# Kernel tuning notes

Hardware: AMD Instinct MI355X
Metric: run time of the kernel (lower is better)

## Reference

```python
import jax, jax.numpy as jnp
import numpy as np

B, S, D, DIM = 8, 4096, 1024, 512  # batch, src nodes, dst nodes, feature dim


def setup_inputs() -> dict:
    key = jax.random.key(0)
    k1, k2, k3, k4, k5 = jax.random.split(key, 5)
    scale = 1.0 / np.sqrt(DIM)
    return {
        "src_val": jax.random.normal(k1, (B, S, DIM), dtype=jnp.float32),
        "src_state": jax.random.normal(k2, (B, S), dtype=jnp.float32),
        "dst_val": jax.random.normal(k3, (B, D, DIM), dtype=jnp.float32),
        "W_route": jax.random.normal(k4, (DIM, DIM), dtype=jnp.float32) * scale,
        "W_val": jax.random.normal(k5, (DIM, DIM), dtype=jnp.float32) * scale,
    }


def reference(src_val, src_state, dst_val, W_route, W_val):
    # Pairwise route logits: bilinear bipartite attention, [B, S, D]
    inv_sqrt_d = 1.0 / jnp.sqrt(jnp.asarray(src_val.shape[-1], src_val.dtype))
    q = jnp.einsum("bsd,de->bse", src_val, W_route)
    logits = jnp.einsum("bse,bke->bsk", q, dst_val) * inv_sqrt_d
    # route compression: softmax over dst nodes (dim=-1)
    routes = jax.nn.softmax(logits, axis=-1)
    # projections
    projected_val = jnp.einsum("bsd,de->bse", src_val, W_val)  # [B, S, DIM]
    projected_state = src_state                                 # identity state proj, [B, S]
    sender_strength = jax.nn.softplus(src_state)                # [B, S]
    # weighted routing + accumulation
    weighted_routes = routes * sender_strength[..., None]       # [B, S, D]
    delta_state = jnp.einsum("bsk,bs->bk", weighted_routes, projected_state)   # [B, D]
    delta_val = jnp.einsum("bsk,bsd->bkd", weighted_routes, projected_val)     # [B, D, DIM]
    return delta_state, delta_val
```

## Files before the change

kernel.cpp:

```cpp
#include <hip/hip_runtime.h>
#include <hip/hip_fp16.h>

#define B_   8
#define S_   4096
#define DD_  1024
#define DIM_ 512
#define SCALE 0.044194173824159216f

typedef __bf16 bf16x8 __attribute__((ext_vector_type(8)));
typedef float  floatx4 __attribute__((ext_vector_type(4)));

__device__ inline unsigned short f2bf(float f) {
    union { float f; unsigned int u; } v; v.f = f;
    unsigned int r = v.u + 0x7fffu + ((v.u >> 16) & 1u);
    return (unsigned short)(r >> 16);
}
__device__ inline float bf2f(unsigned short h) {
    union { unsigned int u; float f; } v; v.u = ((unsigned int)h) << 16;
    return v.f;
}
__device__ inline uint4 cvt8(const float* __restrict__ g) {
    float4 f0 = *(const float4*)g;
    float4 f1 = *(const float4*)(g + 4);
    unsigned short tmp[8] = {f2bf(f0.x), f2bf(f0.y), f2bf(f0.z), f2bf(f0.w),
                             f2bf(f1.x), f2bf(f1.y), f2bf(f1.z), f2bf(f1.w)};
    return *(const uint4*)tmp;
}
__device__ inline void async16(unsigned short* lds, const unsigned short* g) {
    __builtin_amdgcn_global_load_lds(
        (const __attribute__((address_space(1))) void*)g,
        (__attribute__((address_space(3))) void*)lds, 16, 0, 0);
}

template <int AF32, int BF32>
__device__ inline void mainloop(unsigned short* As, unsigned short* Bs,
                                const void* Ap, size_t lda,
                                const void* Bp, size_t ldb,
                                int kIters, floatx4 (&acc)[4][4]) {
    const int t = threadIdx.x, lane = t & 63, wave = t >> 6;
    const int rA = t >> 2, cA = (t & 3) * 8;
    const int mrow = (wave >> 1) * 64, ncol = (wave & 1) * 64;
    const int fr = lane & 15, fk = (lane >> 4) * 8;

    const unsigned short* gA16 = nullptr; const float* gA32 = nullptr;
    const unsigned short* gB16 = nullptr; const float* gB32 = nullptr;
    if (AF32) gA32 = (const float*)Ap + (size_t)rA * lda + cA;
    else      gA16 = (const unsigned short*)Ap + (size_t)rA * lda + cA;
    if (BF32) gB32 = (const float*)Bp + (size_t)rA * ldb + cA;
    else      gB16 = (const unsigned short*)Bp + (size_t)rA * ldb + cA;

    unsigned short* ldsA = As + wave * 512;
    unsigned short* ldsB = Bs + wave * 512;

    for (int kt = 0; kt < kIters; ++kt) {
        if (AF32) {
            *(uint4*)&As[t * 8]        = cvt8(gA32);
            *(uint4*)&As[2048 + t * 8] = cvt8(gA32 + 64 * lda);
            gA32 += 32;
        } else {
            async16(ldsA,        gA16);
            async16(ldsA + 2048, gA16 + 64 * lda);
            gA16 += 32;
        }
        if (BF32) {
            *(uint4*)&Bs[t * 8]        = cvt8(gB32);
            *(uint4*)&Bs[2048 + t * 8] = cvt8(gB32 + 64 * ldb);
            gB32 += 32;
        } else {
            async16(ldsB,        gB16);
            async16(ldsB + 2048, gB16 + 64 * ldb);
            gB16 += 32;
        }
        __syncthreads();
        bf16x8 af[4], bfr[4];
#pragma unroll
        for (int i = 0; i < 4; ++i)
            af[i] = *(const bf16x8*)&As[(mrow + i * 16 + fr) * 32 + fk];
#pragma unroll
        for (int j = 0; j < 4; ++j)
            bfr[j] = *(const bf16x8*)&Bs[(ncol + j * 16 + fr) * 32 + fk];
#pragma unroll
        for (int i = 0; i < 4; ++i)
#pragma unroll
            for (int j = 0; j < 4; ++j)
                acc[i][j] = __builtin_amdgcn_mfma_f32_16x16x32_bf16(af[i], bfr[j],
                                                                    acc[i][j], 0, 0, 0);
        __syncthreads();
    }
}

#define EPILOGUE_COORDS                                     \
    const int lane = threadIdx.x & 63, wave = threadIdx.x >> 6; \
    const int mrow = (wave >> 1) * 64, ncol = (wave & 1) * 64;  \
    const int col = lane & 15, q = lane >> 4;

#define ACC_INIT                                            \
    floatx4 acc[4][4];                                      \
    _Pragma("unroll") for (int i = 0; i < 4; ++i)           \
        _Pragma("unroll") for (int j = 0; j < 4; ++j)       \
            acc[i][j] = (floatx4){0.f, 0.f, 0.f, 0.f};

__global__ __launch_bounds__(256) void k_prep(const float* __restrict__ src,
                                              unsigned short* __restrict__ srcb,
                                              const float* __restrict__ dst,
                                              unsigned short* __restrict__ dstb) {
    const int t = threadIdx.x;
    if (blockIdx.x < 8192) {
        const size_t idx = ((size_t)blockIdx.x * 256 + t) * 8;
        *(uint4*)&srcb[idx] = cvt8(src + idx);
    } else {
        const size_t idx = ((size_t)(blockIdx.x - 8192) * 256 + t) * 8;
        *(uint4*)&dstb[idx] = cvt8(dst + idx);
    }
}

__global__ __launch_bounds__(256) void k_dstWr(const unsigned short* __restrict__ dstb,
                                               const float* __restrict__ Wr,
                                               unsigned short* __restrict__ DW) {
    __shared__ unsigned short As[128 * 32];
    __shared__ unsigned short Bs[128 * 32];
    const int n0 = blockIdx.x * 128, m0 = blockIdx.y * 128;
    ACC_INIT
    mainloop<0, 1>(As, Bs, dstb + (size_t)m0 * DIM_, DIM_,
                   Wr + (size_t)n0 * DIM_, DIM_, DIM_ / 32, acc);
    EPILOGUE_COORDS
#pragma unroll
    for (int i = 0; i < 4; ++i)
#pragma unroll
        for (int j = 0; j < 4; ++j)
#pragma unroll
            for (int r = 0; r < 4; ++r)
                DW[(size_t)(m0 + mrow + i * 16 + q * 4 + r) * DIM_ +
                   n0 + ncol + j * 16 + col] = f2bf(acc[i][j][r] * SCALE);
}

__global__ __launch_bounds__(256) void k_logitsT(const unsigned short* __restrict__ DW,
                                                 const unsigned short* __restrict__ srcb,
                                                 unsigned short* __restrict__ LTb,
                                                 float* __restrict__ Lpart) {
    __shared__ unsigned short As[128 * 32];
    __shared__ unsigned short Bs[128 * 32];
    __shared__ float csum[8][128];
    const int n = blockIdx.x;
    const int b = n & 7;
    const int rem = n >> 3;
    const int xs = rem >> 3;
    const int yd = rem & 7;
    const int n0 = xs * 128, m0 = yd * 128;
    ACC_INIT
    mainloop<0, 0>(As, Bs,
                   DW + (size_t)b * DD_ * DIM_ + (size_t)m0 * DIM_, DIM_,
                   srcb + (size_t)b * S_ * DIM_ + (size_t)n0 * DIM_, DIM_,
                   DIM_ / 32, acc);
    EPILOGUE_COORDS
    unsigned short* LT = LTb + (size_t)b * DD_ * S_;
    float psum[4] = {0.f, 0.f, 0.f, 0.f};
#pragma unroll
    for (int i = 0; i < 4; ++i)
#pragma unroll
        for (int j = 0; j < 4; ++j)
#pragma unroll
            for (int r = 0; r < 4; ++r) {
                float e = __expf(acc[i][j][r]);
                LT[(size_t)(m0 + mrow + i * 16 + q * 4 + r) * S_ +
                   n0 + ncol + j * 16 + col] = f2bf(e);
                psum[j] += e;
            }
    const int slice = (wave >> 1) * 4 + q;
#pragma unroll
    for (int j = 0; j < 4; ++j) csum[slice][ncol + j * 16 + col] = psum[j];
    __syncthreads();
    const int t = threadIdx.x;
    if (t < 128) {
        float v = 0.f;
#pragma unroll
        for (int k = 0; k < 8; ++k) v += csum[k][t];
        Lpart[((size_t)b * 8 + yd) * S_ + n0 + t] = v;
    }
}

__global__ __launch_bounds__(256) void k_finalize(const float* __restrict__ state,
                                                  const float* __restrict__ Lpart,
                                                  float* __restrict__ scale) {
    const int i = blockIdx.x * 256 + threadIdx.x;
    const int b = i >> 12, s = i & (S_ - 1);
    float d = 0.f;
#pragma unroll
    for (int k = 0; k < 8; ++k) d += Lpart[((size_t)b * 8 + k) * S_ + s];
    const float st = state[i];
    const float sp = (st > 15.f) ? st : log1pf(__expf(st));
    scale[i] = sp / d;
}

__global__ __launch_bounds__(256) void k_srcT(const unsigned short* __restrict__ srcb,
                                              const float* __restrict__ scale,
                                              unsigned short* __restrict__ srcST) {
    __shared__ unsigned short Ts[64 * 65];
    const int s0 = blockIdx.x * 64, d0 = blockIdx.y * 64, b = blockIdx.z;
    const int t = threadIdx.x;
    {
        const int r = t >> 2, c0 = (t & 3) * 16;
        const unsigned short* g =
            srcb + (size_t)b * S_ * DIM_ + (size_t)(s0 + r) * DIM_ + d0 + c0;
        uint4 v0 = *(const uint4*)g;
        uint4 v1 = *(const uint4*)(g + 8);
        const unsigned short* e0 = (const unsigned short*)&v0;
        const unsigned short* e1 = (const unsigned short*)&v1;
        const float sc = scale[(size_t)b * S_ + s0 + r];
#pragma unroll
        for (int i = 0; i < 8; ++i) {
            Ts[r * 65 + c0 + i]     = f2bf(bf2f(e0[i]) * sc);
            Ts[r * 65 + c0 + 8 + i] = f2bf(bf2f(e1[i]) * sc);
        }
    }
    __syncthreads();
    {
        const int rr = t >> 2, c0 = (t & 3) * 16;
        unsigned short tmp[16];
#pragma unroll
        for (int j = 0; j < 16; ++j) tmp[j] = Ts[(c0 + j) * 65 + rr];
        unsigned short* o =
            srcST + (size_t)b * DIM_ * S_ + (size_t)(d0 + rr) * S_ + s0 + c0;
        *(uint4*)o = *(const uint4*)tmp;
        *(uint4*)(o + 8) = *(const uint4*)(tmp + 8);
    }
}

__global__ __launch_bounds__(256) void k_dstate(const unsigned short* __restrict__ LT,
                                                const float* __restrict__ state,
                                                const float* __restrict__ scale,
                                                float* __restrict__ out) {
    const int b = blockIdx.y;
    const int dd = blockIdx.x * 4 + (threadIdx.x >> 6);
    const int lane = threadIdx.x & 63;
    const unsigned short* row = LT + (size_t)b * DD_ * S_ + (size_t)dd * S_;
    const float* st = state + (size_t)b * S_;
    const float* sc = scale + (size_t)b * S_;

    float acc = 0.f;
#pragma unroll
    for (int it = 0; it < S_ / 512; ++it) {
        const int s = it * 512 + lane * 8;
        uint4 v = *(const uint4*)(row + s);
        const unsigned short* e = (const unsigned short*)&v;
        float4 f0 = *(const float4*)(st + s);
        float4 f1 = *(const float4*)(st + s + 4);
        float4 c0 = *(const float4*)(sc + s);
        float4 c1 = *(const float4*)(sc + s + 4);
        acc += bf2f(e[0]) * f0.x * c0.x + bf2f(e[1]) * f0.y * c0.y +
               bf2f(e[2]) * f0.z * c0.z + bf2f(e[3]) * f0.w * c0.w +
               bf2f(e[4]) * f1.x * c1.x + bf2f(e[5]) * f1.y * c1.y +
               bf2f(e[6]) * f1.z * c1.z + bf2f(e[7]) * f1.w * c1.w;
    }
#pragma unroll
    for (int off = 32; off; off >>= 1) acc += __shfl_down(acc, off);
    if (lane == 0) out[(size_t)b * DD_ + dd] = acc;
}

__global__ __launch_bounds__(256) void k_dU(const unsigned short* __restrict__ LTb,
                                            const unsigned short* __restrict__ srcST,
                                            __half* __restrict__ Pp) {
    __shared__ unsigned short As[128 * 32];
    __shared__ unsigned short Bs[128 * 32];
    const int n = blockIdx.x;
    const int z = (n & 7) + 8 * (n >> 8);
    const int rem = (n >> 3) & 31;
    const int xe = rem >> 3;
    const int yd = rem & 7;
    const int b = z >> 2, ks = z & 3;
    const int n0 = xe * 128, m0 = yd * 128;
    ACC_INIT
    mainloop<0, 0>(As, Bs,
                   LTb + (size_t)b * DD_ * S_ + (size_t)m0 * S_ + ks * 1024, S_,
                   srcST + (size_t)b * DIM_ * S_ + (size_t)n0 * S_ + ks * 1024, S_,
                   1024 / 32, acc);
    EPILOGUE_COORDS
    __half* O = Pp + (size_t)ks * B_ * DD_ * DIM_ + (size_t)b * DD_ * DIM_;
#pragma unroll
    for (int i = 0; i < 4; ++i)
#pragma unroll
        for (int j = 0; j < 4; ++j)
#pragma unroll
            for (int r = 0; r < 4; ++r)
                O[(size_t)(m0 + mrow + i * 16 + q * 4 + r) * DIM_ +
                  n0 + ncol + j * 16 + col] = __float2half(acc[i][j][r]);
}

__global__ __launch_bounds__(256) void k_reduceU(const __half* __restrict__ Pp,
                                                 unsigned short* __restrict__ U,
                                                 const float* __restrict__ Wv,
                                                 unsigned short* __restrict__ WvT) {
    __shared__ float Ts[64 * 68];
    const int t = threadIdx.x;
    if (blockIdx.x < 2048) {
        const size_t idx = ((size_t)blockIdx.x * 256 + t) * 8;
        const size_t n = (size_t)B_ * DD_ * DIM_;
        float o[8] = {0.f, 0.f, 0.f, 0.f, 0.f, 0.f, 0.f, 0.f};
#pragma unroll
        for (int ks = 0; ks < 4; ++ks) {
            uint4 v = *(const uint4*)(Pp + (size_t)ks * n + idx);
            const __half* h = (const __half*)&v;
#pragma unroll
            for (int j = 0; j < 8; ++j) o[j] += __half2float(h[j]);
        }
        unsigned short tmp[8];
#pragma unroll
        for (int j = 0; j < 8; ++j) tmp[j] = f2bf(o[j]);
        *(uint4*)&U[idx] = *(const uint4*)tmp;
        return;
    }
    const int n2 = blockIdx.x - 2048;
    const int d0 = (n2 & 7) * 64, e0 = (n2 >> 3) * 64;
    {
        const int r = t >> 2, c0 = (t & 3) * 16;
        const float* g = Wv + (size_t)(d0 + r) * DIM_ + e0 + c0;
#pragma unroll
        for (int i = 0; i < 4; ++i)
            *(float4*)&Ts[r * 68 + c0 + i * 4] = *(const float4*)(g + i * 4);
    }
    __syncthreads();
    {
        const int rr = t >> 2, c0 = (t & 3) * 16;
        unsigned short tmp[16];
#pragma unroll
        for (int j = 0; j < 16; ++j) tmp[j] = f2bf(Ts[(c0 + j) * 68 + rr]);
        unsigned short* o = WvT + (size_t)(e0 + rr) * DIM_ + d0 + c0;
        *(uint4*)o = *(const uint4*)tmp;
        *(uint4*)(o + 8) = *(const uint4*)(tmp + 8);
    }
}

__global__ __launch_bounds__(256) void k_dvalW(const unsigned short* __restrict__ U,
                                               const unsigned short* __restrict__ WvT,
                                               float* __restrict__ d_val) {
    __shared__ unsigned short As[128 * 32];
    __shared__ unsigned short Bs[128 * 32];
    const int n0 = blockIdx.x * 128, m0 = blockIdx.y * 128;
    ACC_INIT
    mainloop<0, 0>(As, Bs, U + (size_t)m0 * DIM_, DIM_,
                   WvT + (size_t)n0 * DIM_, DIM_, DIM_ / 32, acc);
    EPILOGUE_COORDS
#pragma unroll
    for (int i = 0; i < 4; ++i)
#pragma unroll
        for (int j = 0; j < 4; ++j)
#pragma unroll
            for (int r = 0; r < 4; ++r)
                d_val[(size_t)(m0 + mrow + i * 16 + q * 4 + r) * DIM_ +
                      n0 + ncol + j * 16 + col] = acc[i][j][r];
}

extern "C" void kernel_launch(void* const* d_in, const int* in_sizes, int n_in,
                              void* d_out, int out_size, void* d_ws, size_t ws_size,
                              hipStream_t stream) {
    const float* src   = (const float*)d_in[0];
    const float* state = (const float*)d_in[1];
    const float* dst   = (const float*)d_in[2];
    const float* Wr    = (const float*)d_in[3];
    const float* Wv    = (const float*)d_in[4];

    unsigned short* srcb = (unsigned short*)d_ws;
    __half* Pp = (__half*)d_ws;
    unsigned short* LT = srcb + (size_t)B_ * S_ * DIM_;
    unsigned short* U  = LT;
    unsigned short* WvT = U + (size_t)B_ * DD_ * DIM_;
    unsigned short* C = LT + (size_t)B_ * DD_ * S_;
    unsigned short* dstb = C;
    unsigned short* DW = dstb + (size_t)B_ * DD_ * DIM_;
    float* Lpart = (float*)(DW + (size_t)B_ * DD_ * DIM_);
    unsigned short* srcST = C;

    float* d_state = (float*)d_out;
    float* d_val   = (float*)d_out + B_ * DD_;
    float* scale   = d_val;

    k_prep<<<dim3(8192 + 2048), 256, 0, stream>>>(src, srcb, dst, dstb);
    k_dstWr<<<dim3(DIM_ / 128, (B_ * DD_) / 128), 256, 0, stream>>>(dstb, Wr, DW);
    k_logitsT<<<dim3(2048), 256, 0, stream>>>(DW, srcb, LT, Lpart);
    k_finalize<<<dim3((B_ * S_) / 256), 256, 0, stream>>>(state, Lpart, scale);
    k_dstate<<<dim3(DD_ / 4, B_), 256, 0, stream>>>(LT, state, scale, d_state);
    k_srcT<<<dim3(S_ / 64, DIM_ / 64, B_), 256, 0, stream>>>(srcb, scale, srcST);
    k_dU<<<dim3(1024), 256, 0, stream>>>(LT, srcST, Pp);
    k_reduceU<<<dim3(2048 + 64), 256, 0, stream>>>(Pp, U, Wv, WvT);
    k_dvalW<<<dim3(DIM_ / 128, (B_ * DD_) / 128), 256, 0, stream>>>(U, WvT, d_val);
}
```

Before: 303.8 us.

## Double-buffer GEMM LDS tiles, swizzle LDS layout, fuse dst conversion into dstWr

The shared GEMM mainloop now uses two LDS buffers, so the next k-tile is loaded while MFMAs run on the current one, and a single barrier per iteration replaces the two. It also XOR-swizzles the 16-byte column chunk on both the store and fragment-load side to cut LDS bank conflicts. The dst fp32->bf16 pre-conversion pass is dropped; k_dstWr converts dst on the fly, which removes one read-write pass over dst. Doubling LDS per block may lower occupancy. Dropping the trailing barrier is only safe if the loop still syncs once per iteration, and the hidden tail of the loop cannot be checked.

```diff
diff --git a/kernel.cpp b/kernel.cpp
--- a/kernel.cpp
+++ b/kernel.cpp
@@ -38,9 +38,11 @@
                                 const void* Bp, size_t ldb,
                                 int kIters, floatx4 (&acc)[4][4]) {
     const int t = threadIdx.x, lane = t & 63, wave = t >> 6;
-    const int rA = t >> 2, cA = (t & 3) * 8;
+    const int rA = t >> 2;
+    const int cA = ((t & 3) ^ ((t >> 3) & 3)) * 8;
     const int mrow = (wave >> 1) * 64, ncol = (wave & 1) * 64;
     const int fr = lane & 15, fk = (lane >> 4) * 8;
+    const int swz = (((fk >> 3) ^ ((fr >> 1) & 3)) << 3);
 
     const unsigned short* gA16 = nullptr; const float* gA32 = nullptr;
     const unsigned short* gB16 = nullptr; const float* gB32 = nullptr;
@@ -52,33 +54,40 @@
     unsigned short* ldsA = As + wave * 512;
     unsigned short* ldsB = Bs + wave * 512;
 
-    for (int kt = 0; kt < kIters; ++kt) {
+    auto stage = [&](int buf) {
+        const int o = buf * 4096;
         if (AF32) {
-            *(uint4*)&As[t * 8]        = cvt8(gA32);
-            *(uint4*)&As[2048 + t * 8] = cvt8(gA32 + 64 * lda);
+            *(uint4*)&As[o + t * 8]        = cvt8(gA32);
+            *(uint4*)&As[o + 2048 + t * 8] = cvt8(gA32 + 64 * lda);
             gA32 += 32;
         } else {
-            async16(ldsA,        gA16);
-            async16(ldsA + 2048, gA16 + 64 * lda);
+            async16(ldsA + o,        gA16);
+            async16(ldsA + o + 2048, gA16 + 64 * lda);
             gA16 += 32;
         }
         if (BF32) {
-            *(uint4*)&Bs[t * 8]        = cvt8(gB32);
-            *(uint4*)&Bs[2048 + t * 8] = cvt8(gB32 + 64 * ldb);
+            *(uint4*)&Bs[o + t * 8]        = cvt8(gB32);
+            *(uint4*)&Bs[o + 2048 + t * 8] = cvt8(gB32 + 64 * ldb);
             gB32 += 32;
         } else {
-            async16(ldsB,        gB16);
-            async16(ldsB + 2048, gB16 + 64 * ldb);
+            async16(ldsB + o,        gB16);
+            async16(ldsB + o + 2048, gB16 + 64 * ldb);
             gB16 += 32;
         }
-        __syncthreads();
+    };
+
+    stage(0);
+    __syncthreads();
+    for (int kt = 0; kt < kIters; ++kt) {
+        if (kt + 1 < kIters) stage((kt + 1) & 1);
+        const int cur = (kt & 1) * 4096;
         bf16x8 af[4], bfr[4];
 #pragma unroll
         for (int i = 0; i < 4; ++i)
-            af[i] = *(const bf16x8*)&As[(mrow + i * 16 + fr) * 32 + fk];
-#pragma unroll
-        for (int j = 0; j < 4; ++j)
-            bfr[j] = *(const bf16x8*)&Bs[(ncol + j * 16 + fr) * 32 + fk];
+            af[i] = *(const bf16x8*)&As[cur + (mrow + i * 16 + fr) * 32 + swz];
+#pragma unroll
+        for (int j = 0; j < 4; ++j)
+            bfr[j] = *(const bf16x8*)&Bs[cur + (ncol + j * 16 + fr) * 32 + swz];
 #pragma unroll
         for (int i = 0; i < 4; ++i)
 #pragma unroll
@@ -101,27 +110,19 @@
             acc[i][j] = (floatx4){0.f, 0.f, 0.f, 0.f};
 
 __global__ __launch_bounds__(256) void k_prep(const float* __restrict__ src,
-                                              unsigned short* __restrict__ srcb,
-                                              const float* __restrict__ dst,
-                                              unsigned short* __restrict__ dstb) {
-    const int t = threadIdx.x;
-    if (blockIdx.x < 8192) {
-        const size_t idx = ((size_t)blockIdx.x * 256 + t) * 8;
-        *(uint4*)&srcb[idx] = cvt8(src + idx);
-    } else {
-        const size_t idx = ((size_t)(blockIdx.x - 8192) * 256 + t) * 8;
-        *(uint4*)&dstb[idx] = cvt8(dst + idx);
-    }
-}
-
-__global__ __launch_bounds__(256) void k_dstWr(const unsigned short* __restrict__ dstb,
+                                              unsigned short* __restrict__ srcb) {
+    const size_t idx = ((size_t)blockIdx.x * 256 + threadIdx.x) * 8;
+    *(uint4*)&srcb[idx] = cvt8(src + idx);
+}
+
+__global__ __launch_bounds__(256) void k_dstWr(const float* __restrict__ dst,
                                                const float* __restrict__ Wr,
                                                unsigned short* __restrict__ DW) {
-    __shared__ unsigned short As[128 * 32];
-    __shared__ unsigned short Bs[128 * 32];
+    __shared__ unsigned short As[2 * 128 * 32];
+    __shared__ unsigned short Bs[2 * 128 * 32];
     const int n0 = blockIdx.x * 128, m0 = blockIdx.y * 128;
     ACC_INIT
-    mainloop<0, 1>(As, Bs, dstb + (size_t)m0 * DIM_, DIM_,
+    mainloop<1, 1>(As, Bs, dst + (size_t)m0 * DIM_, DIM_,
                    Wr + (size_t)n0 * DIM_, DIM_, DIM_ / 32, acc);
     EPILOGUE_COORDS
 #pragma unroll
@@ -138,8 +139,8 @@
                                                  const unsigned short* __restrict__ srcb,
                                                  unsigned short* __restrict__ LTb,
                                                  float* __restrict__ Lpart) {
-    __shared__ unsigned short As[128 * 32];
-    __shared__ unsigned short Bs[128 * 32];
+    __shared__ unsigned short As[2 * 128 * 32];
+    __shared__ unsigned short Bs[2 * 128 * 32];
     __shared__ float csum[8][128];
     const int n = blockIdx.x;
     const int b = n & 7;
@@ -260,8 +261,8 @@
 __global__ __launch_bounds__(256) void k_dU(const unsigned short* __restrict__ LTb,
                                             const unsigned short* __restrict__ srcST,
                                             __half* __restrict__ Pp) {
-    __shared__ unsigned short As[128 * 32];
-    __shared__ unsigned short Bs[128 * 32];
+    __shared__ unsigned short As[2 * 128 * 32];
+    __shared__ unsigned short Bs[2 * 128 * 32];
     const int n = blockIdx.x;
     const int z = (n & 7) + 8 * (n >> 8);
     const int rem = (n >> 3) & 31;
@@ -333,8 +334,8 @@
 __global__ __launch_bounds__(256) void k_dvalW(const unsigned short* __restrict__ U,
                                                const unsigned short* __restrict__ WvT,
                                                float* __restrict__ d_val) {
-    __shared__ unsigned short As[128 * 32];
-    __shared__ unsigned short Bs[128 * 32];
+    __shared__ unsigned short As[2 * 128 * 32];
+    __shared__ unsigned short Bs[2 * 128 * 32];
     const int n0 = blockIdx.x * 128, m0 = blockIdx.y * 128;
     ACC_INIT
     mainloop<0, 0>(As, Bs, U + (size_t)m0 * DIM_, DIM_,
@@ -365,8 +366,7 @@
     unsigned short* U  = LT;
     unsigned short* WvT = U + (size_t)B_ * DD_ * DIM_;
     unsigned short* C = LT + (size_t)B_ * DD_ * S_;
-    unsigned short* dstb = C;
-    unsigned short* DW = dstb + (size_t)B_ * DD_ * DIM_;
+    unsigned short* DW = C;
     float* Lpart = (float*)(DW + (size_t)B_ * DD_ * DIM_);
     unsigned short* srcST = C;
 
@@ -374,8 +374,8 @@
     float* d_val   = (float*)d_out + B_ * DD_;
     float* scale   = d_val;
 
-    k_prep<<<dim3(8192 + 2048), 256, 0, stream>>>(src, srcb, dst, dstb);
-    k_dstWr<<<dim3(DIM_ / 128, (B_ * DD_) / 128), 256, 0, stream>>>(dstb, Wr, DW);
+    k_prep<<<dim3(8192), 256, 0, stream>>>(src, srcb);
+    k_dstWr<<<dim3(DIM_ / 128, (B_ * DD_) / 128), 256, 0, stream>>>(dst, Wr, DW);
     k_logitsT<<<dim3(2048), 256, 0, stream>>>(DW, srcb, LT, Lpart);
     k_finalize<<<dim3((B_ * S_) / 256), 256, 0, stream>>>(state, Lpart, scale);
     k_dstate<<<dim3(DD_ / 4, B_), 256, 0, stream>>>(LT, state, scale, d_state);
```

After: 289.4 us. -4.7%, faster.
